# Kernel optimization log

Hardware: AMD Instinct MI355X
Metric: run time of the kernel (lower is better)

## Reference

```python
import jax, jax.numpy as jnp
import numpy as np

EPS = 1e-6   # param.eps
DT = 1e-2    # param.dt
DX = 1.0     # param.dx
DY = 1.0     # param.dy
N_PARAM = 1.0  # param.N


def _lap(c, dx=1.0, dy=1.0):
    # 5-point periodic Laplacian stencil on the last two dims
    return ((jnp.roll(c, 1, -1) + jnp.roll(c, -1, -1) - 2.0 * c) / (dx * dx)
            + (jnp.roll(c, 1, -2) + jnp.roll(c, -1, -2) - 2.0 * c) / (dy * dy))


def _log_with_mask(m, eps=EPS):
    # masked positions get constant eps -> zero gradient there, like torch masked_fill
    return jnp.log(jnp.where(m < eps, eps, m))


def setup_inputs() -> dict:
    key = jax.random.key(0)
    ks = jax.random.split(key, 12)
    B, H, W = 8, 1024, 1024
    inp = {
        "cv": jax.random.uniform(ks[0], (B, H, W), dtype=jnp.float32),
        "ci": jax.random.uniform(ks[1], (B, H, W), dtype=jnp.float32),
        "eta": jax.random.uniform(ks[2], (B, H, W), dtype=jnp.float32),
    }
    names = ["energy_v0", "energy_i0", "kBT0", "kappa_v0", "kappa_i0",
             "kappa_eta0", "diff_v0", "diff_i0", "L0"]
    for i, n in enumerate(names):
        inp[n] = jax.random.uniform(ks[3 + i], (1,), dtype=jnp.float32)
    return inp


def reference(cv, ci, eta, energy_v0, energy_i0, kBT0, kappa_v0, kappa_i0,
              kappa_eta0, diff_v0, diff_i0, L0):
    energy_v = jnp.abs(energy_v0) + 0.001
    energy_i = jnp.abs(energy_i0) + 0.001
    kBT = jnp.abs(kBT0) + 0.001
    kappa_v = jnp.abs(kappa_v0) + 0.001
    kappa_i = jnp.abs(kappa_i0) + 0.001
    kappa_eta = jnp.abs(kappa_eta0) + 0.001
    diff_v = jnp.abs(diff_v0) + 0.001
    diff_i = jnp.abs(diff_i0) + 0.001
    L = jnp.abs(L0) + 0.001

    lap_cv = _lap(cv, DX, DY)
    lap_ci = _lap(ci, DX, DY)
    lap_eta = _lap(eta, DX, DY)

    h = (eta - 1.0) ** 2
    j = eta ** 2
    cs = 1.0 - cv - ci
    log_cv = _log_with_mask(cv)
    log_ci = _log_with_mask(ci)
    log_cs = _log_with_mask(cs)

    fs = energy_v * cv + energy_i * ci + kBT * (cv * log_cv + ci * log_ci + cs * log_cs)
    dfs_dcv = energy_v + kBT * (log_cv - log_cs)
    dfs_dci = energy_i + kBT * (log_ci - log_cs)

    fv = (cv - 1.0) ** 2 + ci ** 2
    dfv_dcv = 2.0 * (cv - 1.0)
    dfv_dci = 2.0 * ci

    dF_dcv = h * dfs_dcv + j * dfv_dcv - kappa_v * lap_cv
    dF_dci = h * dfs_dci + j * dfv_dci - kappa_i * lap_ci
    dF_deta = N_PARAM * (fs * 2.0 * (eta - 1.0) + fv * 2.0 * eta - kappa_eta * lap_eta)

    mv = diff_v * cv / kBT
    mi = diff_i * ci / kBT

    cv_new = jnp.clip(cv + DT * (mv * _lap(dF_dcv)), 0.0, 1.0)
    ci_new = jnp.clip(ci + DT * (mi * _lap(dF_dci)), 0.0, 1.0)
    eta_new = jnp.clip(eta + DT * (-L * dF_deta), 0.0, 1.0)
    return cv_new, ci_new, eta_new
```

## Files before the change

kernel.cpp:

```cpp
#include <hip/hip_runtime.h>

#define WMASK 1023
#define LOG2W 10
#define HW (1024 * 1024)

#define EPS 1e-6f
#define DT 1e-2f

#define TX 64
#define TY 16

#define RCH 21
#define RYT 20
#define RST 84
#define FPAD 448

#define DCH 18
#define DYT 18
#define DST 76

typedef float f4 __attribute__((ext_vector_type(4)));

__device__ __forceinline__ float scal(const float* __restrict__ p) {
    return fabsf(p[0]) + 0.001f;
}
__device__ __forceinline__ float logm(float m) {
    return __logf(m < EPS ? EPS : m);
}
__device__ __forceinline__ float clip01(float v) {
    return fminf(fmaxf(v, 0.0f), 1.0f);
}

__global__ __launch_bounds__(256) void irr_fused(
    const float* __restrict__ cv,
    const float* __restrict__ ci,
    const float* __restrict__ eta,
    const float* __restrict__ p_ev,
    const float* __restrict__ p_ei,
    const float* __restrict__ p_kbt,
    const float* __restrict__ p_kv,
    const float* __restrict__ p_ki,
    const float* __restrict__ p_ke,
    const float* __restrict__ p_dv,
    const float* __restrict__ p_di,
    const float* __restrict__ p_L,
    float* __restrict__ cv_new,
    float* __restrict__ ci_new,
    float* __restrict__ eta_new)
{
    __shared__ float scv[RYT][RST];
    __shared__ float sci[RYT][RST];
    __shared__ float seta[RYT][RST];
    __shared__ float sdv[DYT][DST];
    __shared__ float sdi[DYT][DST];

    const int tid = threadIdx.x;
    const int x0 = blockIdx.x * TX;
    const int y0 = blockIdx.y * TY;
    const int bbase = blockIdx.z * HW;

    const float energy_v = scal(p_ev);
    const float energy_i = scal(p_ei);
    const float kBT      = scal(p_kbt);
    const float kappa_v  = scal(p_kv);
    const float kappa_i  = scal(p_ki);
    const float kappa_e  = scal(p_ke);
    const float diff_v   = scal(p_dv);
    const float diff_i   = scal(p_di);
    const float L        = scal(p_L);
    const float rv = diff_v / kBT;
    const float ri = diff_i / kBT;

    for (int t = tid; t < 3 * FPAD; t += 256) {
        const int f = t / FPAD;
        const int r = t - f * FPAD;
        if (r < RCH * RYT) {
            const int cx = r % RCH;
            const int cy = r / RCH;
            const int gx = (x0 - 8 + (cx << 2)) & WMASK;
            const int gy = (y0 - 2 + cy) & WMASK;
            const float* __restrict__ src = (f == 0) ? cv : (f == 1) ? ci : eta;
            const f4 v = *(const f4*)(src + bbase + (gy << LOG2W) + gx);
            float* dst = (f == 0) ? &scv[cy][cx << 2]
                       : (f == 1) ? &sci[cy][cx << 2]
                                  : &seta[cy][cx << 2];
            *(f4*)dst = v;
        }
    }
    __syncthreads();

    for (int t = tid; t < DCH * DYT; t += 256) {
        const int k  = t % DCH;
        const int ey = t / DCH;
        const int rx = (k << 2) + 4;
        const int ry = ey + 1;

        const f4    cC = *(const f4*)&scv[ry][rx];
        const float cL = scv[ry][rx - 1];
        const float cR = scv[ry][rx + 4];
        const f4    cU = *(const f4*)&scv[ry - 1][rx];
        const f4    cD = *(const f4*)&scv[ry + 1][rx];

        const f4    iC = *(const f4*)&sci[ry][rx];
        const float iL = sci[ry][rx - 1];
        const float iR = sci[ry][rx + 4];
        const f4    iU = *(const f4*)&sci[ry - 1][rx];
        const f4    iD = *(const f4*)&sci[ry + 1][rx];

        const f4    eC = *(const f4*)&seta[ry][rx];
        const float eL = seta[ry][rx - 1];
        const float eR = seta[ry][rx + 4];
        const f4    eU = *(const f4*)&seta[ry - 1][rx];
        const f4    eD = *(const f4*)&seta[ry + 1][rx];

        f4 dv, di, en;
        #pragma unroll
        for (int j = 0; j < 4; ++j) {
            const float c0 = cC[j];
            const float i0 = iC[j];
            const float e0 = eC[j];
            const float cl = (j == 0) ? cL : cC[j - 1];
            const float cr = (j == 3) ? cR : cC[j + 1];
            const float il = (j == 0) ? iL : iC[j - 1];
            const float ir = (j == 3) ? iR : iC[j + 1];
            const float el = (j == 0) ? eL : eC[j - 1];
            const float er = (j == 3) ? eR : eC[j + 1];

            const float lap_cv  = cl + cr + cU[j] + cD[j] - 4.0f * c0;
            const float lap_ci  = il + ir + iU[j] + iD[j] - 4.0f * i0;
            const float lap_eta = el + er + eU[j] + eD[j] - 4.0f * e0;

            const float h  = (e0 - 1.0f) * (e0 - 1.0f);
            const float jj = e0 * e0;
            const float cs = 1.0f - c0 - i0;
            const float lgv = logm(c0);
            const float lgi = logm(i0);
            const float lgs = logm(cs);

            const float dfs_dcv = energy_v + kBT * (lgv - lgs);
            const float dfs_dci = energy_i + kBT * (lgi - lgs);

            dv[j] = h * dfs_dcv + jj * (2.0f * (c0 - 1.0f)) - kappa_v * lap_cv;
            di[j] = h * dfs_dci + jj * (2.0f * i0)          - kappa_i * lap_ci;

            const float fs = energy_v * c0 + energy_i * i0
                           + kBT * (c0 * lgv + i0 * lgi + cs * lgs);
            const float fv = (c0 - 1.0f) * (c0 - 1.0f) + i0 * i0;
            const float dF_deta = fs * 2.0f * (e0 - 1.0f) + fv * 2.0f * e0
                                - kappa_e * lap_eta;
            en[j] = clip01(e0 + DT * (-L * dF_deta));
        }

        *(f4*)&sdv[ey][k << 2] = dv;
        *(f4*)&sdi[ey][k << 2] = di;

        if (k >= 1 && k <= 16 && ey >= 1 && ey <= 16) {
            const int gidx = bbase + ((y0 - 1 + ey) << LOG2W)
                           + (x0 - 4 + (k << 2));
            __builtin_nontemporal_store(en, (f4*)(eta_new + gidx));
        }
    }
    __syncthreads();

    {
        const int ox4 = tid & 15;
        const int oy  = tid >> 4;
        const int ex  = (ox4 << 2) + 4;
        const int ey  = oy + 1;

        const f4    vC = *(const f4*)&sdv[ey][ex];
        const float vL = sdv[ey][ex - 1];
        const float vR = sdv[ey][ex + 4];
        const f4    vU = *(const f4*)&sdv[ey - 1][ex];
        const f4    vD = *(const f4*)&sdv[ey + 1][ex];

        const f4    wC = *(const f4*)&sdi[ey][ex];
        const float wL = sdi[ey][ex - 1];
        const float wR = sdi[ey][ex + 4];
        const f4    wU = *(const f4*)&sdi[ey - 1][ex];
        const f4    wD = *(const f4*)&sdi[ey + 1][ex];

        const f4 c0 = *(const f4*)&scv[oy + 2][(ox4 << 2) + 8];
        const f4 i0 = *(const f4*)&sci[oy + 2][(ox4 << 2) + 8];

        const int gidx = bbase + ((y0 + oy) << LOG2W) + (x0 + (ox4 << 2));

        f4 outv, outi;
        #pragma unroll
        for (int j = 0; j < 4; ++j) {
            const float lv = ((j == 0) ? vL : vC[j - 1])
                           + ((j == 3) ? vR : vC[j + 1])
                           + vU[j] + vD[j] - 4.0f * vC[j];
            const float li = ((j == 0) ? wL : wC[j - 1])
                           + ((j == 3) ? wR : wC[j + 1])
                           + wU[j] + wD[j] - 4.0f * wC[j];
            outv[j] = clip01(c0[j] + DT * ((rv * c0[j]) * lv));
            outi[j] = clip01(i0[j] + DT * ((ri * i0[j]) * li));
        }
        __builtin_nontemporal_store(outv, (f4*)(cv_new + gidx));
        __builtin_nontemporal_store(outi, (f4*)(ci_new + gidx));
    }
}

extern "C" void kernel_launch(void* const* d_in, const int* in_sizes, int n_in,
                              void* d_out, int out_size, void* d_ws, size_t ws_size,
                              hipStream_t stream) {
    const float* cv  = (const float*)d_in[0];
    const float* ci  = (const float*)d_in[1];
    const float* eta = (const float*)d_in[2];
    const float* p_ev  = (const float*)d_in[3];
    const float* p_ei  = (const float*)d_in[4];
    const float* p_kbt = (const float*)d_in[5];
    const float* p_kv  = (const float*)d_in[6];
    const float* p_ki  = (const float*)d_in[7];
    const float* p_ke  = (const float*)d_in[8];
    const float* p_dv  = (const float*)d_in[9];
    const float* p_di  = (const float*)d_in[10];
    const float* p_L   = (const float*)d_in[11];

    const int N = in_sizes[0];

    float* out     = (float*)d_out;
    float* cv_new  = out;
    float* ci_new  = out + N;
    float* eta_new = out + 2 * N;

    const dim3 block(256);
    const dim3 grid(1024 / TX, 1024 / TY, N / HW);

    irr_fused<<<grid, block, 0, stream>>>(cv, ci, eta, p_ev, p_ei, p_kbt,
                                          p_kv, p_ki, p_ke, p_dv, p_di, p_L,
                                          cv_new, ci_new, eta_new);
}
```

Before: 215.2 us.

## Trim shared-memory halo and fetch edge columns directly from global memory

The staged input tiles shrink from 21 to 18 float4 columns, and eta drops from 20 to 18 rows. The two outermost halo columns for cv/ci are now read with scalar global loads only by edge threads, and eta's unused halo is replaced with clamped or zero values in positions whose results are discarded. This cuts global load traffic and shared-memory footprint, which may raise occupancy. Logs also switch to log2 with a folded ln2 constant. The tradeoff is extra scattered scalar global loads and divergence at the k==0 and k==17 threads.

New measurement: 212.6 us. No clear change (-1.2%).

```diff
diff --git a/kernel.cpp b/kernel.cpp
--- a/kernel.cpp
+++ b/kernel.cpp
@@ -10,25 +10,22 @@
 #define TX 64
 #define TY 16
 
-#define RCH 21
-#define RYT 20
-#define RST 84
-#define FPAD 448
+#define RCH 18
+#define RST 72
 
 #define DCH 18
 #define DYT 18
-#define DST 76
 
 typedef float f4 __attribute__((ext_vector_type(4)));
 
 __device__ __forceinline__ float scal(const float* __restrict__ p) {
     return fabsf(p[0]) + 0.001f;
 }
-__device__ __forceinline__ float logm(float m) {
-    return __logf(m < EPS ? EPS : m);
-}
 __device__ __forceinline__ float clip01(float v) {
     return fminf(fmaxf(v, 0.0f), 1.0f);
+}
+__device__ __forceinline__ float lg2m(float m) {
+    return __log2f(fmaxf(m, EPS));
 }
 
 __global__ __launch_bounds__(256) void irr_fused(
@@ -48,11 +45,11 @@
     float* __restrict__ ci_new,
     float* __restrict__ eta_new)
 {
-    __shared__ float scv[RYT][RST];
-    __shared__ float sci[RYT][RST];
-    __shared__ float seta[RYT][RST];
-    __shared__ float sdv[DYT][DST];
-    __shared__ float sdi[DYT][DST];
+    __shared__ float scv[20][RST];
+    __shared__ float sci[20][RST];
+    __shared__ float seta[18][RST];
+    __shared__ float sdv[DYT][RST];
+    __shared__ float sdi[DYT][RST];
 
     const int tid = threadIdx.x;
     const int x0 = blockIdx.x * TX;
@@ -70,48 +67,55 @@
     const float L        = scal(p_L);
     const float rv = diff_v / kBT;
     const float ri = diff_i / kBT;
-
-    for (int t = tid; t < 3 * FPAD; t += 256) {
-        const int f = t / FPAD;
-        const int r = t - f * FPAD;
-        if (r < RCH * RYT) {
-            const int cx = r % RCH;
-            const int cy = r / RCH;
-            const int gx = (x0 - 8 + (cx << 2)) & WMASK;
-            const int gy = (y0 - 2 + cy) & WMASK;
-            const float* __restrict__ src = (f == 0) ? cv : (f == 1) ? ci : eta;
-            const f4 v = *(const f4*)(src + bbase + (gy << LOG2W) + gx);
-            float* dst = (f == 0) ? &scv[cy][cx << 2]
-                       : (f == 1) ? &sci[cy][cx << 2]
-                                  : &seta[cy][cx << 2];
-            *(f4*)dst = v;
-        }
+    const float kl = kBT * 0.69314718056f;
+
+    for (int t = tid; t < 1044; t += 256) {
+        const float* __restrict__ src;
+        float (*dstA)[RST];
+        int r, gy0;
+        if (t < 360)      { src = cv;  r = t;       gy0 = y0 - 2; dstA = scv; }
+        else if (t < 720) { src = ci;  r = t - 360; gy0 = y0 - 2; dstA = sci; }
+        else              { src = eta; r = t - 720; gy0 = y0 - 1; dstA = seta; }
+        const int cx = r % RCH;
+        const int cy = r / RCH;
+        const int gx = (x0 - 4 + (cx << 2)) & WMASK;
+        const int gy = (gy0 + cy) & WMASK;
+        const f4 v = *(const f4*)(src + bbase + (gy << LOG2W) + gx);
+        *(f4*)&dstA[cy][cx << 2] = v;
     }
     __syncthreads();
 
     for (int t = tid; t < DCH * DYT; t += 256) {
         const int k  = t % DCH;
         const int ey = t / DCH;
-        const int rx = (k << 2) + 4;
+        const int rx = k << 2;
         const int ry = ey + 1;
 
-        const f4    cC = *(const f4*)&scv[ry][rx];
-        const float cL = scv[ry][rx - 1];
-        const float cR = scv[ry][rx + 4];
-        const f4    cU = *(const f4*)&scv[ry - 1][rx];
-        const f4    cD = *(const f4*)&scv[ry + 1][rx];
-
-        const f4    iC = *(const f4*)&sci[ry][rx];
-        const float iL = sci[ry][rx - 1];
-        const float iR = sci[ry][rx + 4];
-        const f4    iU = *(const f4*)&sci[ry - 1][rx];
-        const f4    iD = *(const f4*)&sci[ry + 1][rx];
-
-        const f4    eC = *(const f4*)&seta[ry][rx];
-        const float eL = seta[ry][rx - 1];
-        const float eR = seta[ry][rx + 4];
-        const f4    eU = *(const f4*)&seta[ry - 1][rx];
-        const f4    eD = *(const f4*)&seta[ry + 1][rx];
+        const f4 cC = *(const f4*)&scv[ry][rx];
+        const f4 cU = *(const f4*)&scv[ry - 1][rx];
+        const f4 cD = *(const f4*)&scv[ry + 1][rx];
+        const f4 iC = *(const f4*)&sci[ry][rx];
+        const f4 iU = *(const f4*)&sci[ry - 1][rx];
+        const f4 iD = *(const f4*)&sci[ry + 1][rx];
+        const f4 eC = *(const f4*)&seta[ey][rx];
+        const int eyU = (ey == 0)  ? 0  : ey - 1;
+        const int eyD = (ey == 17) ? 17 : ey + 1;
+        const f4 eU = *(const f4*)&seta[eyU][rx];
+        const f4 eD = *(const f4*)&seta[eyD][rx];
+
+        float cL, cR, iL, iR, eL, eR;
+        if (k == 0) {
+            const int gofs = bbase + (((y0 - 1 + ey) & WMASK) << LOG2W) + ((x0 - 5) & WMASK);
+            cL = cv[gofs]; iL = ci[gofs]; eL = 0.0f;
+        } else {
+            cL = scv[ry][rx - 1]; iL = sci[ry][rx - 1]; eL = seta[ey][rx - 1];
+        }
+        if (k == DCH - 1) {
+            const int gofs = bbase + (((y0 - 1 + ey) & WMASK) << LOG2W) + ((x0 + 68) & WMASK);
+            cR = cv[gofs]; iR = ci[gofs]; eR = 0.0f;
+        } else {
+            cR = scv[ry][rx + 4]; iR = sci[ry][rx + 4]; eR = seta[ey][rx + 4];
+        }
 
         f4 dv, di, en;
         #pragma unroll
@@ -133,26 +137,26 @@
             const float h  = (e0 - 1.0f) * (e0 - 1.0f);
             const float jj = e0 * e0;
             const float cs = 1.0f - c0 - i0;
-            const float lgv = logm(c0);
-            const float lgi = logm(i0);
-            const float lgs = logm(cs);
-
-            const float dfs_dcv = energy_v + kBT * (lgv - lgs);
-            const float dfs_dci = energy_i + kBT * (lgi - lgs);
+            const float lgv = lg2m(c0);
+            const float lgi = lg2m(i0);
+            const float lgs = lg2m(cs);
+
+            const float dfs_dcv = energy_v + kl * (lgv - lgs);
+            const float dfs_dci = energy_i + kl * (lgi - lgs);
 
             dv[j] = h * dfs_dcv + jj * (2.0f * (c0 - 1.0f)) - kappa_v * lap_cv;
             di[j] = h * dfs_dci + jj * (2.0f * i0)          - kappa_i * lap_ci;
 
             const float fs = energy_v * c0 + energy_i * i0
-                           + kBT * (c0 * lgv + i0 * lgi + cs * lgs);
+                           + kl * (c0 * lgv + i0 * lgi + cs * lgs);
             const float fv = (c0 - 1.0f) * (c0 - 1.0f) + i0 * i0;
             const float dF_deta = fs * 2.0f * (e0 - 1.0f) + fv * 2.0f * e0
                                 - kappa_e * lap_eta;
             en[j] = clip01(e0 + DT * (-L * dF_deta));
         }
 
-        *(f4*)&sdv[ey][k << 2] = dv;
-        *(f4*)&sdi[ey][k << 2] = di;
+        *(f4*)&sdv[ey][rx] = dv;
+        *(f4*)&sdi[ey][rx] = di;
 
         if (k >= 1 && k <= 16 && ey >= 1 && ey <= 16) {
             const int gidx = bbase + ((y0 - 1 + ey) << LOG2W)
@@ -180,8 +184,8 @@
         const f4    wU = *(const f4*)&sdi[ey - 1][ex];
         const f4    wD = *(const f4*)&sdi[ey + 1][ex];
 
-        const f4 c0 = *(const f4*)&scv[oy + 2][(ox4 << 2) + 8];
-        const f4 i0 = *(const f4*)&sci[oy + 2][(ox4 << 2) + 8];
+        const f4 c0 = *(const f4*)&scv[oy + 2][ex];
+        const f4 i0 = *(const f4*)&sci[oy + 2][ex];
 
         const int gidx = bbase + ((y0 + oy) << LOG2W) + (x0 + (ox4 << 2));
 
```
